# Kernel tuning notes

Hardware: AMD Instinct MI355X
Metric: run time of the kernel (lower is better)

Reference implementation:

```python
import math
import jax, jax.numpy as jnp
import numpy as np

D_HEAD = 64
KS = 7
EPS = 1e-6


def _rope_freqs(d_head, n_heads):
    # AxialRoPE buffer: exp(linspace(log(pi), log(10*pi), nh*dim//4+1)[:-1]).view(dim//4, nh).T
    dim = d_head // 2
    n = n_heads * dim // 4
    f = np.exp(np.linspace(math.log(math.pi), math.log(10.0 * math.pi), n + 1)[:-1]).astype(np.float32)
    return jnp.asarray(f.reshape(dim // 4, n_heads).T)  # [nh, dim//4]


def setup_inputs() -> dict:
    key = jax.random.key(0)
    ks = jax.random.split(key, 6)
    B, C, T, H, W = 1, 512, 4, 32, 32
    cond_features = 256
    nh = C // D_HEAD
    x = jax.random.normal(ks[0], (B, C, T, H, W), dtype=jnp.float32)
    pos = jax.random.uniform(ks[1], (B, H, W, 2), dtype=jnp.float32)
    cond = jax.random.normal(ks[2], (B, cond_features), dtype=jnp.float32)
    # zero-init layers in the original (norm.linear, out_proj) get small random weights
    # here so the reference exercises nontrivial math/gradients.
    norm_w = jax.random.normal(ks[3], (cond_features, C), dtype=jnp.float32) * 0.02
    qkv_w = jax.random.normal(ks[4], (C, 3 * C), dtype=jnp.float32) * (1.0 / math.sqrt(C))
    out_w = jax.random.normal(ks[5], (C, C), dtype=jnp.float32) * (1.0 / math.sqrt(C))
    scale = jnp.full((nh,), 10.0, dtype=jnp.float32)
    return {"x": x, "pos": pos, "cond": cond, "norm_w": norm_w, "qkv_w": qkv_w,
            "scale": scale, "out_w": out_w}


def reference(x, pos, cond, norm_w, qkv_w, scale, out_w):
    B, C, T, H, W = x.shape
    nh = C // D_HEAD
    N = B * T
    skip = x

    # b c t h w -> (b t) h w c
    xr = jnp.transpose(x, (0, 2, 3, 4, 1)).reshape(N, H, W, C)
    condr = jnp.repeat(cond, T, axis=0)  # (b t) c, b-major

    # AdaRMSNorm: scale = linear(cond) + 1, applied with rms normalization
    s = condr @ norm_w + 1.0  # [N, C]
    mean_sq = jnp.mean(xr * xr, axis=-1, keepdims=True)
    xn = xr * (s[:, None, None, :] * jax.lax.rsqrt(mean_sq + EPS))

    qkv = (xn @ qkv_w).reshape(N, H, W, 3, nh, D_HEAD)
    q, k, v = qkv[:, :, :, 0], qkv[:, :, :, 1], qkv[:, :, :, 2]  # [N,H,W,nh,e]

    # cosine-sim scaling per head
    sqrt_scale = jnp.sqrt(scale)[:, None]  # [nh,1]
    q = q * (sqrt_scale * jax.lax.rsqrt(jnp.sum(q * q, -1, keepdims=True) + EPS))
    k = k * (sqrt_scale * jax.lax.rsqrt(jnp.sum(k * k, -1, keepdims=True) + EPS))

    # axial RoPE
    freqs = _rope_freqs(D_HEAD, nh)  # [nh, e//8]
    theta = jnp.concatenate([pos[..., None, 0:1] * freqs,
                             pos[..., None, 1:2] * freqs], axis=-1)  # [B,H,W,nh,e//4]
    theta = jnp.repeat(theta, T, axis=0)  # [N,H,W,nh,d]
    d = theta.shape[-1]
    cos_t, sin_t = jnp.cos(theta), jnp.sin(theta)

    def rope(t):
        x1, x2, x3 = t[..., :d], t[..., d:2 * d], t[..., 2 * d:]
        return jnp.concatenate([x1 * cos_t - x2 * sin_t,
                                x2 * cos_t + x1 * sin_t, x3], axis=-1)

    q, k = rope(q), rope(k)

    # neighborhood attention (NATTEN na2d semantics: window clamped to image border)
    r = KS // 2
    ih = jnp.clip(jnp.arange(H) - r, 0, H - KS)[:, None] + jnp.arange(KS)  # [H,KS]
    iw = jnp.clip(jnp.arange(W) - r, 0, W - KS)[:, None] + jnp.arange(KS)  # [W,KS]

    def windows(t):  # [N,H,W,nh,e] -> [N,H,W,KS*KS,nh,e]
        g = t[:, ih[:, :, None, None], iw[None, None, :, :]]  # [N,H,KS,W,KS,nh,e]
        return jnp.transpose(g, (0, 1, 3, 2, 4, 5, 6)).reshape(N, H, W, KS * KS, nh, D_HEAD)

    kw, vw = windows(k), windows(v)
    logits = jnp.einsum('nhwce,nhwkce->nhwck', q, kw)  # scale=1.0 in na2d call
    attn = jax.nn.softmax(logits, axis=-1)
    o = jnp.einsum('nhwck,nhwkce->nhwce', attn, vw).reshape(N, H, W, C)

    y = o @ out_w  # dropout=0.0
    y = jnp.transpose(y.reshape(B, T, H, W, C), (0, 4, 1, 2, 3))
    return y + skip
```

## Files before the change

### kernel.cpp

```cpp
#include <hip/hip_runtime.h>
#include <hip/hip_bf16.h>

typedef __hip_bfloat16 bf16;
#define B16(f) __float2bfloat16(f)

typedef __attribute__((ext_vector_type(8))) short short8;
typedef __attribute__((ext_vector_type(4))) float f32x4;

#define P_DIM 4096
#define AS   72

__global__ __launch_bounds__(256) void k_pre(const float* __restrict__ x,
                                             const float* __restrict__ cond,
                                             const float* __restrict__ norm_w,
                                             const float* __restrict__ qkv_w,
                                             const float* __restrict__ out_w,
                                             bf16* __restrict__ qkvT,
                                             bf16* __restrict__ outT,
                                             bf16* __restrict__ xt,
                                             float* __restrict__ rms_part){
  __shared__ float sh[64 * 65];
  __shared__ float s_red[4][64];
  __shared__ float s_sh[64];
  int bid = blockIdx.x;
  int tid = threadIdx.x;
  int grp = tid >> 6, lane = tid & 63;

  if (bid < 192){
    int n0 = (bid % 24) * 64, c0 = (bid / 24) * 64;
    float acc = 0.f;
    for (int f = grp * 64; f < grp * 64 + 64; ++f)
      acc = fmaf(cond[f], norm_w[f * 512 + c0 + lane], acc);
    s_red[grp][lane] = acc;
    for (int i = grp; i < 64; i += 4)
      sh[i * 65 + lane] = qkv_w[(c0 + i) * 1536 + n0 + lane];
    __syncthreads();
    if (tid < 64)
      s_sh[tid] = s_red[0][tid] + s_red[1][tid] + s_red[2][tid] + s_red[3][tid] + 1.0f;
    __syncthreads();
    for (int j = grp; j < 64; j += 4)
      qkvT[(n0 + j) * 512 + c0 + lane] = B16(sh[lane * 65 + j] * s_sh[lane]);
  } else if (bid < 256){
    int bb = bid - 192;
    int n0 = (bb & 7) * 64, c0 = (bb >> 3) * 64;
    for (int i = grp; i < 64; i += 4)
      sh[i * 65 + lane] = out_w[(c0 + i) * 512 + n0 + lane];
    __syncthreads();
    for (int j = grp; j < 64; j += 4)
      outT[(n0 + j) * 512 + c0 + lane] = B16(sh[lane * 65 + j]);
  } else if (bid < 768){
    int b = bid - 256;
    int bp = b & 63, bc = b >> 6;
    int p0 = bp * 64, c0 = bc * 64;
    for (int i = grp; i < 64; i += 4)
      sh[i * 65 + lane] = x[(c0 + i) * P_DIM + p0 + lane];
    __syncthreads();
    for (int j = grp; j < 64; j += 4)
      xt[(size_t)(p0 + j) * 512 + c0 + lane] = B16(sh[lane * 65 + j]);
  } else {
    int b = bid - 768;
    int bp = b & 63, bc = b >> 6;
    int co = tid >> 6, pl = tid & 63;
    int p = bp * 64 + pl;
    float acc = 0.f;
    for (int c = bc * 64 + co; c < bc * 64 + 64; c += 4){
      float v = x[c * P_DIM + p];
      acc = fmaf(v, v, acc);
    }
    sh[co * 64 + pl] = acc;
    __syncthreads();
    if (tid < 64)
      rms_part[bc * P_DIM + bp * 64 + tid] = sh[tid] + sh[64 + tid] + sh[128 + tid] + sh[192 + tid];
  }
}

__global__ __launch_bounds__(256) void k_gemm_qkv(const bf16* __restrict__ Ab,
                                                  const bf16* __restrict__ BTb,
                                                  const float* __restrict__ scale,
                                                  const float* __restrict__ pos,
                                                  const float* __restrict__ rms_part,
                                                  bf16* __restrict__ qkv_bf){
  __shared__ unsigned short a_t[128 * AS];
  __shared__ unsigned short b_t[64 * AS];
  const unsigned short* A  = (const unsigned short*)Ab;
  const unsigned short* BT = (const unsigned short*)BTb;
  int m0 = blockIdx.x * 128;
  int by = blockIdx.y;
  int n0 = by * 64;
  int tid = threadIdx.x;
  int w = tid >> 6, l = tid & 63, g = l >> 4, cb = l & 15;

  f32x4 acc[2][4];
#pragma unroll
  for (int mi = 0; mi < 2; ++mi)
#pragma unroll
    for (int nj = 0; nj < 4; ++nj)
#pragma unroll
      for (int r = 0; r < 4; ++r) acc[mi][nj][r] = 0.f;

  for (int kk = 0; kk < 512; kk += 64){
#pragma unroll
    for (int i = 0; i < 4; ++i){
      int sid = tid + i * 256;
      int row = sid >> 3, seg = sid & 7;
      *(uint4*)&a_t[row * AS + seg * 8] = *(const uint4*)&A[(size_t)(m0 + row) * 512 + kk + seg * 8];
    }
#pragma unroll
    for (int i = 0; i < 2; ++i){
      int sid = tid + i * 256;
      int row = sid >> 3, seg = sid & 7;
      *(uint4*)&b_t[row * AS + seg * 8] = *(const uint4*)&BT[(size_t)(n0 + row) * 512 + kk + seg * 8];
    }
    __syncthreads();
#pragma unroll
    for (int kc = 0; kc < 2; ++kc){
      short8 af[2];
#pragma unroll
      for (int mi = 0; mi < 2; ++mi)
        af[mi] = *(const short8*)&a_t[(w * 32 + mi * 16 + cb) * AS + kc * 32 + g * 8];
#pragma unroll
      for (int nj = 0; nj < 4; ++nj){
        short8 bfr = *(const short8*)&b_t[(nj * 16 + cb) * AS + kc * 32 + g * 8];
#pragma unroll
        for (int mi = 0; mi < 2; ++mi)
          acc[mi][nj] = __builtin_amdgcn_mfma_f32_16x16x32_bf16(af[mi], bfr, acc[mi][nj], 0, 0, 0);
      }
    }
    __syncthreads();
  }

  if (by < 16){
    int head = by & 7;
    float sqs = sqrtf(scale[head]);
    int axis = cb >> 3, fi = cb & 7;
    const float LOG_PI = 1.1447298858494002f;
    const float LOG10F = 2.302585092994046f;
    float f = __expf(LOG_PI + (float)(fi * 8 + head) * (LOG10F / 64.0f));
#pragma unroll
    for (int mi = 0; mi < 2; ++mi)
#pragma unroll
      for (int r = 0; r < 4; ++r){
        float ss = 0.f;
#pragma unroll
        for (int nj = 0; nj < 4; ++nj) ss = fmaf(acc[mi][nj][r], acc[mi][nj][r], ss);
#pragma unroll
        for (int off = 1; off < 16; off <<= 1) ss += __shfl_xor(ss, off, 64);
        float fac = sqs * rsqrtf(ss + 1e-6f);
        int rowg = m0 + w * 32 + mi * 16 + g * 4 + r;
        float th = pos[(rowg & 1023) * 2 + axis] * f;
        float ct = __cosf(th), st = __sinf(th);
        float v0 = acc[mi][0][r] * fac, v1 = acc[mi][1][r] * fac;
        acc[mi][0][r] = v0 * ct - v1 * st;
        acc[mi][1][r] = v1 * ct + v0 * st;
        acc[mi][2][r] *= fac;
        acc[mi][3][r] *= fac;
      }
  } else {
#pragma unroll
    for (int mi = 0; mi < 2; ++mi)
#pragma unroll
      for (int r = 0; r < 4; ++r){
        int rowg = m0 + w * 32 + mi * 16 + g * 4 + r;
        float ss = 0.f;
#pragma unroll
        for (int i = 0; i < 8; ++i) ss += rms_part[i * P_DIM + rowg];
        float rv = rsqrtf(ss * (1.0f / 512.0f) + 1e-6f);
#pragma unroll
        for (int nj = 0; nj < 4; ++nj) acc[mi][nj][r] *= rv;
      }
  }

#pragma unroll
  for (int mi = 0; mi < 2; ++mi)
#pragma unroll
    for (int nj = 0; nj < 4; ++nj){
      int col = n0 + nj * 16 + cb;
#pragma unroll
      for (int r = 0; r < 4; ++r){
        int rowg = m0 + w * 32 + mi * 16 + g * 4 + r;
        qkv_bf[(size_t)rowg * 1536 + col] = B16(acc[mi][nj][r]);
      }
    }
}

#define KL_S 80
#define VT_S 232
#define PP_S 232
__global__ __launch_bounds__(256) void k_attn(const bf16* __restrict__ qkv_bfp,
                                              bf16* __restrict__ o_bf){
  __shared__ unsigned short kp[208 * KL_S];
  __shared__ unsigned short vT[64 * VT_S];
  const unsigned short* qkv = (const unsigned short*)qkv_bfp;

  int bid = blockIdx.x;
  int head = bid & 7;
  int patch = bid >> 3;
  int t = patch >> 4;
  int ph = (patch >> 2) & 3, pw = patch & 3;
  int h0 = ph * 8, w0 = pw * 8;
  int rs = min(max(h0 - 3, 0), 18);
  int cs = min(max(w0 - 3, 0), 18);
  int tbase = t << 10;
  int tid = threadIdx.x;
  int cp = tid & 31, pxg = tid >> 5;

  for (int i = 0; i < 26; ++i){
    int px = i * 8 + pxg;
    unsigned val = 0;
    if (px < 196){
      int rr = px / 14, cc = px - rr * 14;
      size_t pn = (size_t)(tbase + (rs + rr) * 32 + (cs + cc));
      val = *(const unsigned*)&qkv[pn * 1536 + 512 + head * 64 + cp * 2];
    }
    *(unsigned*)&kp[px * KL_S + cp * 2] = val;
  }
  for (int i = 0; i < 14; ++i){
    int pp = i * 8 + pxg;
    int px0 = 2 * pp, px1 = px0 + 1;
    unsigned v0 = 0, v1 = 0;
    if (px0 < 196){
      int rr = px0 / 14, cc = px0 - rr * 14;
      size_t pn = (size_t)(tbase + (rs + rr) * 32 + (cs + cc));
      v0 = *(const unsigned*)&qkv[pn * 1536 + 1024 + head * 64 + cp * 2];
    }
    if (px1 < 196){
      int rr = px1 / 14, cc = px1 - rr * 14;
      size_t pn = (size_t)(tbase + (rs + rr) * 32 + (cs + cc));
      v1 = *(const unsigned*)&qkv[pn * 1536 + 1024 + head * 64 + cp * 2];
    }
    unsigned lo = (v0 & 0xffffu) | (v1 << 16);
    unsigned hi = (v0 >> 16) | (v1 & 0xffff0000u);
    *(unsigned*)&vT[(2 * cp) * VT_S + 2 * pp] = lo;
    *(unsigned*)&vT[(2 * cp + 1) * VT_S + 2 * pp] = hi;
  }

  int w = tid >> 6, l = tid & 63;
  int g = l >> 4, cb = l & 15;

  int q_a = w * 16 + cb;
  size_t abase = (size_t)(tbase + (h0 + (q_a >> 3)) * 32 + (w0 + (q_a & 7))) * 1536 + head * 64;
  short8 qa0 = *(const short8*)&qkv[abase + g * 8];
  short8 qa1 = *(const short8*)&qkv[abase + 32 + g * 8];

  __syncthreads();

  f32x4 acc[13];
#pragma unroll
  for (int nt = 0; nt < 13; ++nt)
#pragma unroll
    for (int r = 0; r < 4; ++r) acc[nt][r] = 0.f;
#pragma unroll
  for (int nt = 0; nt < 13; ++nt){
    short8 kb0 = *(const short8*)&kp[(nt * 16 + cb) * KL_S + g * 8];
    short8 kb1 = *(const short8*)&kp[(nt * 16 + cb) * KL_S + 32 + g * 8];
    acc[nt] = __builtin_amdgcn_mfma_f32_16x16x32_bf16(qa0, kb0, acc[nt], 0, 0, 0);
    acc[nt] = __builtin_amdgcn_mfma_f32_16x16x32_bf16(qa1, kb1, acc[nt], 0, 0, 0);
  }
  __syncthreads();

  int wr0[4], wc0[4];
#pragma unroll
  for (int r = 0; r < 4; ++r){
    int q_l = w * 16 + g * 4 + r;
    int hq = h0 + (q_l >> 3), wq = w0 + (q_l & 7);
    wr0[r] = min(max(hq - 3, 0), 25) - rs;
    wc0[r] = min(max(wq - 3, 0), 25) - cs;
  }
  float mx[4] = {-1e30f, -1e30f, -1e30f, -1e30f};
#pragma unroll
  for (int nt = 0; nt < 13; ++nt){
    int kg = nt * 16 + cb;
    int kr = kg / 14, kc = kg - kr * 14;
    bool kvalid = kg < 196;
#pragma unroll
    for (int r = 0; r < 4; ++r){
      bool v = kvalid && ((unsigned)(kr - wr0[r]) < 7u) && ((unsigned)(kc - wc0[r]) < 7u);
      float lg = v ? acc[nt][r] : -1e30f;
      acc[nt][r] = lg;
      mx[r] = fmaxf(mx[r], lg);
    }
  }
#pragma unroll
  for (int off = 1; off < 16; off <<= 1)
#pragma unroll
    for (int r = 0; r < 4; ++r) mx[r] = fmaxf(mx[r], __shfl_xor(mx[r], off, 64));
  float sm[4] = {0.f, 0.f, 0.f, 0.f};
#pragma unroll
  for (int nt = 0; nt < 13; ++nt)
#pragma unroll
    for (int r = 0; r < 4; ++r){
      float e = __expf(acc[nt][r] - mx[r]);
      acc[nt][r] = e;
      sm[r] += e;
    }
#pragma unroll
  for (int off = 1; off < 16; off <<= 1)
#pragma unroll
    for (int r = 0; r < 4; ++r) sm[r] += __shfl_xor(sm[r], off, 64);
  float inv[4];
#pragma unroll
  for (int r = 0; r < 4; ++r) inv[r] = 1.0f / sm[r];

#pragma unroll
  for (int nt = 0; nt < 13; ++nt)
#pragma unroll
    for (int r = 0; r < 4; ++r)
      *reinterpret_cast<bf16*>(&kp[(w * 16 + g * 4 + r) * PP_S + nt * 16 + cb]) = B16(acc[nt][r] * inv[r]);
#pragma unroll
  for (int r = 0; r < 4; ++r)
    kp[(w * 16 + g * 4 + r) * PP_S + 208 + cb] = 0;
  __syncthreads();

  f32x4 acc2[4];
#pragma unroll
  for (int ct = 0; ct < 4; ++ct)
#pragma unroll
    for (int r = 0; r < 4; ++r) acc2[ct][r] = 0.f;
#pragma unroll
  for (int kt = 0; kt < 7; ++kt){
    short8 pa = *(const short8*)&kp[(w * 16 + cb) * PP_S + kt * 32 + g * 8];
#pragma unroll
    for (int ct = 0; ct < 4; ++ct){
      short8 vb = *(const short8*)&vT[(ct * 16 + cb) * VT_S + kt * 32 + g * 8];
      acc2[ct] = __builtin_amdgcn_mfma_f32_16x16x32_bf16(pa, vb, acc2[ct], 0, 0, 0);
    }
  }
#pragma unroll
  for (int ct = 0; ct < 4; ++ct)
#pragma unroll
    for (int r = 0; r < 4; ++r){
      int q_l = w * 16 + g * 4 + r;
      int p = tbase + (h0 + (q_l >> 3)) * 32 + (w0 + (q_l & 7));
      o_bf[(size_t)p * 512 + head * 64 + ct * 16 + cb] = B16(acc2[ct][r]);
    }
}

__global__ __launch_bounds__(256) void k_gemm_out(const bf16* __restrict__ Ab,
                                                  const bf16* __restrict__ BTb,
                                                  const float* __restrict__ xres,
                                                  float* __restrict__ out){
  __shared__ unsigned short a_t[128 * AS];
  __shared__ unsigned short b_t[64 * AS];
  __shared__ float tile[64][65];
  const unsigned short* A  = (const unsigned short*)Ab;
  const unsigned short* BT = (const unsigned short*)BTb;
  int m0 = blockIdx.x * 128;
  int n0 = blockIdx.y * 64;
  int tid = threadIdx.x;
  int w = tid >> 6, l = tid & 63, g = l >> 4, cb = l & 15;

  f32x4 acc[2][4];
#pragma unroll
  for (int mi = 0; mi < 2; ++mi)
#pragma unroll
    for (int nj = 0; nj < 4; ++nj)
#pragma unroll
      for (int r = 0; r < 4; ++r) acc[mi][nj][r] = 0.f;

  for (int kk = 0; kk < 512; kk += 64){
#pragma unroll
    for (int i = 0; i < 4; ++i){
      int sid = tid + i * 256;
      int row = sid >> 3, seg = sid & 7;
      *(uint4*)&a_t[row * AS + seg * 8] = *(const uint4*)&A[(size_t)(m0 + row) * 512 + kk + seg * 8];
    }
#pragma unroll
    for (int i = 0; i < 2; ++i){
      int sid = tid + i * 256;
      int row = sid >> 3, seg = sid & 7;
      *(uint4*)&b_t[row * AS + seg * 8] = *(const uint4*)&BT[(size_t)(n0 + row) * 512 + kk + seg * 8];
    }
    __syncthreads();
#pragma unroll
    for (int kc = 0; kc < 2; ++kc){
      short8 af[2];
#pragma unroll
      for (int mi = 0; mi < 2; ++mi)
        af[mi] = *(const short8*)&a_t[(w * 32 + mi * 16 + cb) * AS + kc * 32 + g * 8];
#pragma unroll
      for (int nj = 0; nj < 4; ++nj){
        short8 bfr = *(const short8*)&b_t[(nj * 16 + cb) * AS + kc * 32 + g * 8];
#pragma unroll
        for (int mi = 0; mi < 2; ++mi)
          acc[mi][nj] = __builtin_amdgcn_mfma_f32_16x16x32_bf16(af[mi], bfr, acc[mi][nj], 0, 0, 0);
      }
    }
    __syncthreads();
  }
  int grp = tid >> 6, lane = tid & 63;
#pragma unroll
  for (int hh = 0; hh < 2; ++hh){
    __syncthreads();
    if ((w >> 1) == hh){
#pragma unroll
      for (int mi = 0; mi < 2; ++mi)
#pragma unroll
        for (int nj = 0; nj < 4; ++nj)
#pragma unroll
          for (int r = 0; r < 4; ++r)
            tile[(w & 1) * 32 + mi * 16 + g * 4 + r][nj * 16 + cb] = acc[mi][nj][r];
    }
    __syncthreads();
    for (int j2 = grp; j2 < 64; j2 += 4){
      int c = n0 + j2;
      int p = m0 + hh * 64 + lane;
      out[(size_t)c * P_DIM + p] = tile[lane][j2] + xres[(size_t)c * P_DIM + p];
    }
  }
}

extern "C" void kernel_launch(void* const* d_in, const int* in_sizes, int n_in,
                              void* d_out, int out_size, void* d_ws, size_t ws_size,
                              hipStream_t stream){
  const float* x      = (const float*)d_in[0];
  const float* pos    = (const float*)d_in[1];
  const float* cond   = (const float*)d_in[2];
  const float* norm_w = (const float*)d_in[3];
  const float* qkv_w  = (const float*)d_in[4];
  const float* scale  = (const float*)d_in[5];
  const float* out_w  = (const float*)d_in[6];
  float* out = (float*)d_out;

  char* wp = (char*)d_ws;
  auto alloc = [&](size_t bytes) -> char* {
    char* r = wp;
    wp += (bytes + 255) & ~((size_t)255);
    return r;
  };
  float* rms_part = (float*)alloc(8 * 4096 * 4);
  bf16*  xt       = (bf16*) alloc((size_t)4096 * 512 * 2);
  bf16*  qkvT     = (bf16*) alloc((size_t)1536 * 512 * 2);
  bf16*  outT     = (bf16*) alloc((size_t)512 * 512 * 2);
  bf16*  qkv_bf   = (bf16*) alloc((size_t)4096 * 1536 * 2);
  bf16*  o_bf     = (bf16*) alloc((size_t)4096 * 512 * 2);

  k_pre     <<<1280,        256, 0, stream>>>(x, cond, norm_w, qkv_w, out_w,
                                              qkvT, outT, xt, rms_part);
  k_gemm_qkv<<<dim3(32,24), 256, 0, stream>>>(xt, qkvT, scale, pos, rms_part, qkv_bf);
  k_attn    <<<512,         256, 0, stream>>>(qkv_bf, o_bf);
  k_gemm_out<<<dim3(32,8),  256, 0, stream>>>(o_bf, outT, x, out);
}
```

Baseline: 133.3 us.

## Fuse RMS partials into x transpose, register-prefetch GEMM tiles, shrink out-GEMM tile

The pre-kernel now computes the per-pixel sum of squares while it loads x for the bf16 transpose, which removes a second full read of x and 512 blocks. Both GEMMs now prefetch the next K-slice into registers before the MFMA loop, so global loads overlap compute. The output GEMM tile drops from 128 to 64 rows, doubling the grid to 512 blocks for better occupancy and a simpler epilogue. The cost is more register pressure and more B-tile reloads.

```diff
diff --git a/kernel.cpp b/kernel.cpp
--- a/kernel.cpp
+++ b/kernel.cpp
@@ -20,7 +20,7 @@
                                              bf16* __restrict__ xt,
                                              float* __restrict__ rms_part){
   __shared__ float sh[64 * 65];
-  __shared__ float s_red[4][64];
+  __shared__ float red[4][64];
   __shared__ float s_sh[64];
   int bid = blockIdx.x;
   int tid = threadIdx.x;
@@ -31,12 +31,12 @@
     float acc = 0.f;
     for (int f = grp * 64; f < grp * 64 + 64; ++f)
       acc = fmaf(cond[f], norm_w[f * 512 + c0 + lane], acc);
-    s_red[grp][lane] = acc;
+    red[grp][lane] = acc;
     for (int i = grp; i < 64; i += 4)
       sh[i * 65 + lane] = qkv_w[(c0 + i) * 1536 + n0 + lane];
     __syncthreads();
     if (tid < 64)
-      s_sh[tid] = s_red[0][tid] + s_red[1][tid] + s_red[2][tid] + s_red[3][tid] + 1.0f;
+      s_sh[tid] = red[0][tid] + red[1][tid] + red[2][tid] + red[3][tid] + 1.0f;
     __syncthreads();
     for (int j = grp; j < 64; j += 4)
       qkvT[(n0 + j) * 512 + c0 + lane] = B16(sh[lane * 65 + j] * s_sh[lane]);
@@ -48,29 +48,22 @@
     __syncthreads();
     for (int j = grp; j < 64; j += 4)
       outT[(n0 + j) * 512 + c0 + lane] = B16(sh[lane * 65 + j]);
-  } else if (bid < 768){
+  } else {
     int b = bid - 256;
     int bp = b & 63, bc = b >> 6;
     int p0 = bp * 64, c0 = bc * 64;
-    for (int i = grp; i < 64; i += 4)
-      sh[i * 65 + lane] = x[(c0 + i) * P_DIM + p0 + lane];
-    __syncthreads();
+    float a2 = 0.f;
+    for (int i = grp; i < 64; i += 4){
+      float v = x[(c0 + i) * P_DIM + p0 + lane];
+      sh[i * 65 + lane] = v;
+      a2 = fmaf(v, v, a2);
+    }
+    red[grp][lane] = a2;
+    __syncthreads();
+    if (tid < 64)
+      rms_part[bc * P_DIM + p0 + tid] = red[0][tid] + red[1][tid] + red[2][tid] + red[3][tid];
     for (int j = grp; j < 64; j += 4)
       xt[(size_t)(p0 + j) * 512 + c0 + lane] = B16(sh[lane * 65 + j]);
-  } else {
-    int b = bid - 768;
-    int bp = b & 63, bc = b >> 6;
-    int co = tid >> 6, pl = tid & 63;
-    int p = bp * 64 + pl;
-    float acc = 0.f;
-    for (int c = bc * 64 + co; c < bc * 64 + 64; c += 4){
-      float v = x[c * P_DIM + p];
-      acc = fmaf(v, v, acc);
-    }
-    sh[co * 64 + pl] = acc;
-    __syncthreads();
-    if (tid < 64)
-      rms_part[bc * P_DIM + bp * 64 + tid] = sh[tid] + sh[64 + tid] + sh[128 + tid] + sh[192 + tid];
   }
 }
 
@@ -89,6 +82,7 @@
   int n0 = by * 64;
   int tid = threadIdx.x;
   int w = tid >> 6, l = tid & 63, g = l >> 4, cb = l & 15;
+  int sr = tid >> 3, seg = tid & 7;
 
   f32x4 acc[2][4];
 #pragma unroll
@@ -98,20 +92,30 @@
 #pragma unroll
       for (int r = 0; r < 4; ++r) acc[mi][nj][r] = 0.f;
 
+  uint4 ra[4], rb[2];
+#pragma unroll
+  for (int i = 0; i < 4; ++i)
+    ra[i] = *(const uint4*)&A[(size_t)(m0 + sr + 32 * i) * 512 + seg * 8];
+#pragma unroll
+  for (int i = 0; i < 2; ++i)
+    rb[i] = *(const uint4*)&BT[(size_t)(n0 + sr + 32 * i) * 512 + seg * 8];
+
   for (int kk = 0; kk < 512; kk += 64){
 #pragma unroll
-    for (int i = 0; i < 4; ++i){
-      int sid = tid + i * 256;
-      int row = sid >> 3, seg = sid & 7;
-      *(uint4*)&a_t[row * AS + seg * 8] = *(const uint4*)&A[(size_t)(m0 + row) * 512 + kk + seg * 8];
-    }
-#pragma unroll
-    for (int i = 0; i < 2; ++i){
-      int sid = tid + i * 256;
-      int row = sid >> 3, seg = sid & 7;
-      *(uint4*)&b_t[row * AS + seg * 8] = *(const uint4*)&BT[(size_t)(n0 + row) * 512 + kk + seg * 8];
-    }
-    __syncthreads();
+    for (int i = 0; i < 4; ++i)
+      *(uint4*)&a_t[(sr + 32 * i) * AS + seg * 8] = ra[i];
+#pragma unroll
+    for (int i = 0; i < 2; ++i)
+      *(uint4*)&b_t[(sr + 32 * i) * AS + seg * 8] = rb[i];
+    __syncthreads();
+    if (kk < 448){
+#pragma unroll
+      for (int i = 0; i < 4; ++i)
+        ra[i] = *(const uint4*)&A[(size_t)(m0 + sr + 32 * i) * 512 + kk + 64 + seg * 8];
+#pragma unroll
+      for (int i = 0; i < 2; ++i)
+        rb[i] = *(const uint4*)&BT[(size_t)(n0 + sr + 32 * i) * 512 + kk + 64 + seg * 8];
+    }
 #pragma unroll
     for (int kc = 0; kc < 2; ++kc){
       short8 af[2];
@@ -339,73 +343,66 @@
                                                   const bf16* __restrict__ BTb,
                                                   const float* __restrict__ xres,
                                                   float* __restrict__ out){
-  __shared__ unsigned short a_t[128 * AS];
+  __shared__ unsigned short a_t[64 * AS];
   __shared__ unsigned short b_t[64 * AS];
   __shared__ float tile[64][65];
   const unsigned short* A  = (const unsigned short*)Ab;
   const unsigned short* BT = (const unsigned short*)BTb;
-  int m0 = blockIdx.x * 128;
+  int m0 = blockIdx.x * 64;
   int n0 = blockIdx.y * 64;
   int tid = threadIdx.x;
   int w = tid >> 6, l = tid & 63, g = l >> 4, cb = l & 15;
-
-  f32x4 acc[2][4];
-#pragma unroll
-  for (int mi = 0; mi < 2; ++mi)
-#pragma unroll
-    for (int nj = 0; nj < 4; ++nj)
-#pragma unroll
-      for (int r = 0; r < 4; ++r) acc[mi][nj][r] = 0.f;
+  int sr = tid >> 3, seg = tid & 7;
+
+  f32x4 acc[4];
+#pragma unroll
+  for (int nj = 0; nj < 4; ++nj)
+#pragma unroll
+    for (int r = 0; r < 4; ++r) acc[nj][r] = 0.f;
+
+  uint4 ra[2], rb[2];
+#pragma unroll
+  for (int i = 0; i < 2; ++i){
+    ra[i] = *(const uint4*)&A[(size_t)(m0 + sr + 32 * i) * 512 + seg * 8];
+    rb[i] = *(const uint4*)&BT[(size_t)(n0 + sr + 32 * i) * 512 + seg * 8];
+  }
 
   for (int kk = 0; kk < 512; kk += 64){
 #pragma unroll
-    for (int i = 0; i < 4; ++i){
-      int sid = tid + i * 256;
-      int row = sid >> 3, seg = sid & 7;
-      *(uint4*)&a_t[row * AS + seg * 8] = *(const uint4*)&A[(size_t)(m0 + row) * 512 + kk + seg * 8];
-    }
-#pragma unroll
     for (int i = 0; i < 2; ++i){
-      int sid = tid + i * 256;
-      int row = sid >> 3, seg = sid & 7;
-      *(uint4*)&b_t[row * AS + seg * 8] = *(const uint4*)&BT[(size_t)(n0 + row) * 512 + kk + seg * 8];
-    }
-    __syncthreads();
+      *(uint4*)&a_t[(sr + 32 * i) * AS + seg * 8] = ra[i];
+      *(uint4*)&b_t[(sr + 32 * i) * AS + seg * 8] = rb[i];
+    }
+    __syncthreads();
+    if (kk < 448){
+#pragma unroll
+      for (int i = 0; i < 2; ++i){
+        ra[i] = *(const uint4*)&A[(size_t)(m0 + sr + 32 * i) * 512 + kk + 64 + seg * 8];
+        rb[i] = *(const uint4*)&BT[(size_t)(n0 + sr + 32 * i) * 512 + kk + 64 + seg * 8];
+      }
+    }
 #pragma unroll
     for (int kc = 0; kc < 2; ++kc){
-      short8 af[2];
-#pragma unroll
-      for (int mi = 0; mi < 2; ++mi)
-        af[mi] = *(const short8*)&a_t[(w * 32 + mi * 16 + cb) * AS + kc * 32 + g * 8];
+      short8 af = *(const short8*)&a_t[(w * 16 + cb) * AS + kc * 32 + g * 8];
 #pragma unroll
       for (int nj = 0; nj < 4; ++nj){
         short8 bfr = *(const short8*)&b_t[(nj * 16 + cb) * AS + kc * 32 + g * 8];
-#pragma unroll
-        for (int mi = 0; mi < 2; ++mi)
-          acc[mi][nj] = __builtin_amdgcn_mfma_f32_16x16x32_bf16(af[mi], bfr, acc[mi][nj], 0, 0, 0);
-      }
-    }
-    __syncthreads();
-  }
+        acc[nj] = __builtin_amdgcn_mfma_f32_16x16x32_bf16(af, bfr, acc[nj], 0, 0, 0);
+      }
+    }
+    __syncthreads();
+  }
+#pragma unroll
+  for (int nj = 0; nj < 4; ++nj)
+#pragma unroll
+    for (int r = 0; r < 4; ++r)
+      tile[w * 16 + g * 4 + r][nj * 16 + cb] = acc[nj][r];
+  __syncthreads();
   int grp = tid >> 6, lane = tid & 63;
-#pragma unroll
-  for (int hh = 0; hh < 2; ++hh){
-    __syncthreads();
-    if ((w >> 1) == hh){
-#pragma unroll
-      for (int mi = 0; mi < 2; ++mi)
-#pragma unroll
-        for (int nj = 0; nj < 4; ++nj)
-#pragma unroll
-          for (int r = 0; r < 4; ++r)
-            tile[(w & 1) * 32 + mi * 16 + g * 4 + r][nj * 16 + cb] = acc[mi][nj][r];
-    }
-    __syncthreads();
-    for (int j2 = grp; j2 < 64; j2 += 4){
-      int c = n0 + j2;
-      int p = m0 + hh * 64 + lane;
-      out[(size_t)c * P_DIM + p] = tile[lane][j2] + xres[(size_t)c * P_DIM + p];
-    }
+  for (int j2 = grp; j2 < 64; j2 += 4){
+    int c = n0 + j2;
+    int p = m0 + lane;
+    out[(size_t)c * P_DIM + p] = tile[lane][j2] + xres[(size_t)c * P_DIM + p];
   }
 }
 
@@ -434,9 +431,9 @@
   bf16*  qkv_bf   = (bf16*) alloc((size_t)4096 * 1536 * 2);
   bf16*  o_bf     = (bf16*) alloc((size_t)4096 * 512 * 2);
 
-  k_pre     <<<1280,        256, 0, stream>>>(x, cond, norm_w, qkv_w, out_w,
+  k_pre     <<<768,         256, 0, stream>>>(x, cond, norm_w, qkv_w, out_w,
                                               qkvT, outT, xt, rms_part);
   k_gemm_qkv<<<dim3(32,24), 256, 0, stream>>>(xt, qkvT, scale, pos, rms_part, qkv_bf);
   k_attn    <<<512,         256, 0, stream>>>(qkv_bf, o_bf);
-  k_gemm_out<<<dim3(32,8),  256, 0, stream>>>(o_bf, outT, x, out);
+  k_gemm_out<<<dim3(64,8),  256, 0, stream>>>(o_bf, outT, x, out);
 }
```

Measured after the change: 172.5 us. 1.29x slower.
